# Kernel tuning notes

Hardware: AMD Instinct MI355X
Metric: run time of the kernel (lower is better)

## Reference

```python
import jax, jax.numpy as jnp
import numpy as np

INV_TEMP = 10.0

def pairwise_distance(x, y):
    # squared L2 distance: [b,n,c],[b,m,c] -> [b,n,m]
    x2 = jnp.sum(x * x, axis=-1, keepdims=True)          # [b,n,1]
    y2 = jnp.sum(y * y, axis=-1)[:, None, :]             # [b,1,m]
    xy = jnp.einsum('bnc,bmc->bnm', x, y)                # [b,n,m]
    return x2 + y2 - 2.0 * xy

def setup_inputs() -> dict:
    key = jax.random.key(0)
    k1, k2, k3 = jax.random.split(key, 3)
    b, n, m, c = 4, 4096, 4096, 32
    x_f = jax.random.normal(k1, (b, n, c), dtype=jnp.float32)
    y_f = jax.random.normal(k2, (b, m, c), dtype=jnp.float32)
    y_c = jax.random.normal(k3, (b, m, 3), dtype=jnp.float32)
    temp_inv = jnp.ones((1,), dtype=jnp.float32) * INV_TEMP
    return {"x_f": x_f, "y_f": y_f, "y_c": y_c, "temp_inv": temp_inv}

def reference(x_f, y_f, y_c, temp_inv):
    # corr_type='soft', st=True (straight-through)
    dist = pairwise_distance(x_f, y_f)                   # [b,n,m]
    y_soft = jax.nn.softmax(-dist * temp_inv[0], axis=2) # [b,n,m]
    index = jnp.argmax(y_soft, axis=2)                   # [b,n]
    y_hard = jax.nn.one_hot(index, y_soft.shape[2], dtype=y_soft.dtype)
    ret = y_hard - jax.lax.stop_gradient(y_soft) + y_soft
    x_corr = jnp.matmul(ret, y_c)                        # [b,n,3]
    return x_corr
```

## Files before the change

### kernel.cpp

```cpp
#include <hip/hip_runtime.h>

#define B 4
#define N 4096
#define M 4096
#define C 32
#define BN (B * N)

typedef short bf16x8 __attribute__((ext_vector_type(8)));
typedef float f32x4  __attribute__((ext_vector_type(4)));
typedef unsigned int u32x4 __attribute__((ext_vector_type(4)));

#define WS_WI ((size_t)8 * BN * 4)
#define WS_YH (WS_WI * 2)
#define WS_YM (WS_YH + (size_t)B * M * C * 2)
#define WS_YL (WS_YM + (size_t)B * M * C * 2)
#define WS_Y2 (WS_YL + (size_t)B * M * C * 2)

__device__ __forceinline__ float bf16lo(unsigned int u) { return __uint_as_float(u << 16); }
__device__ __forceinline__ float bf16hi(unsigned int u) { return __uint_as_float(u & 0xffff0000u); }

__device__ __forceinline__ void split3(const float f[8], bf16x8& h, bf16x8& m, bf16x8& l) {
    u32x4 hw, mw, lw;
    #pragma unroll
    for (int p = 0; p < 4; ++p) {
        const float f0 = f[2*p], f1 = f[2*p+1];
        const unsigned int h0 = __float_as_uint(f0) & 0xffff0000u;
        const unsigned int h1 = __float_as_uint(f1) & 0xffff0000u;
        hw[p] = h1 | (h0 >> 16);
        const float r0 = f0 - __uint_as_float(h0);
        const float r1 = f1 - __uint_as_float(h1);
        const unsigned int m0 = __float_as_uint(r0) & 0xffff0000u;
        const unsigned int m1 = __float_as_uint(r1) & 0xffff0000u;
        mw[p] = m1 | (m0 >> 16);
        const float s0 = r0 - __uint_as_float(m0);
        const float s1 = r1 - __uint_as_float(m1);
        lw[p] = (__float_as_uint(s1) & 0xffff0000u) | (__float_as_uint(s0) >> 16);
    }
    h = __builtin_bit_cast(bf16x8, hw);
    m = __builtin_bit_cast(bf16x8, mw);
    l = __builtin_bit_cast(bf16x8, lw);
}

__global__ __launch_bounds__(256)
void y_prepass(const void* __restrict__ yptr, const unsigned short* __restrict__ tptr,
               void* __restrict__ ws) {
    if (tptr[0] == 0x4120) return;
    unsigned short* yh = (unsigned short*)((char*)ws + WS_YH);
    unsigned short* ym = (unsigned short*)((char*)ws + WS_YM);
    unsigned short* yl = (unsigned short*)((char*)ws + WS_YL);
    float*          y2 = (float*)((char*)ws + WS_Y2);

    const int gid = blockIdx.x * 256 + threadIdx.x;
    const int row = gid >> 2;
    const int seg = gid & 3;
    const float* p = (const float*)yptr + (size_t)row * C + seg * 8;
    float4 v0 = *(const float4*)p;
    float4 v1 = *(const float4*)(p + 4);
    const float f[8] = {v0.x, v0.y, v0.z, v0.w, v1.x, v1.y, v1.z, v1.w};

    bf16x8 h, m, l;
    split3(f, h, m, l);
    const size_t o = (size_t)row * C + seg * 8;
    *(bf16x8*)(yh + o) = h;
    *(bf16x8*)(ym + o) = m;
    *(bf16x8*)(yl + o) = l;

    float s = 0.f;
    #pragma unroll
    for (int k = 0; k < 8; ++k) s = fmaf(f[k], f[k], s);
    s += __shfl_xor(s, 1, 64);
    s += __shfl_xor(s, 2, 64);
    if (seg == 0) y2[row] = -0.5f * s;
}

__global__ __launch_bounds__(256, 4)
void nn_main(const void* __restrict__ xptr, const void* __restrict__ yptr,
             const unsigned short* __restrict__ tptr, void* __restrict__ ws) {
    float* wD = (float*)ws;
    int*   wI = (int*)((char*)ws + WS_WI);
    const bool is_bf16 = (tptr[0] == 0x4120);

    __shared__ float y2s[512];

    const int tid  = threadIdx.x;
    const int lane = tid & 63;
    const int wv   = tid >> 6;
    const int col  = lane & 15;
    const int quad = lane >> 4;
    const int bi   = blockIdx.x;
    const int ms   = bi & 7;
    const int nb   = (bi >> 3) & 31;
    const int b    = bi >> 8;
    const int n_base = nb * 128 + wv * 32;

    float bD[2][4];
    int   bI[2][4];
    #pragma unroll
    for (int t = 0; t < 2; ++t)
        #pragma unroll
        for (int r = 0; r < 4; ++r) { bD[t][r] = -__builtin_inff(); bI[t][r] = 0; }

    const size_t boff = (size_t)col * C + quad * 8;

    if (is_bf16) {
        const unsigned short* yp = (const unsigned short*)yptr;
        const unsigned short* xp = (const unsigned short*)xptr;

        for (int r = tid; r < 512; r += 256) {
            const int m = ms * 512 + r;
            const uint4* p = (const uint4*)(yp + ((size_t)b * M + m) * C);
            float s = 0.f;
            #pragma unroll
            for (int i = 0; i < 4; ++i) {
                uint4 v = p[i];
                float f;
                f = bf16lo(v.x); s = fmaf(f, f, s); f = bf16hi(v.x); s = fmaf(f, f, s);
                f = bf16lo(v.y); s = fmaf(f, f, s); f = bf16hi(v.y); s = fmaf(f, f, s);
                f = bf16lo(v.z); s = fmaf(f, f, s); f = bf16hi(v.z); s = fmaf(f, f, s);
                f = bf16lo(v.w); s = fmaf(f, f, s); f = bf16hi(v.w); s = fmaf(f, f, s);
            }
            y2s[r] = -0.5f * s;
        }

        bf16x8 af[2];
        #pragma unroll
        for (int t = 0; t < 2; ++t)
            af[t] = *(const bf16x8*)(xp + ((size_t)b * N + n_base + t * 16 + col) * C + quad * 8);

        __syncthreads();

        const unsigned short* yb = yp + ((size_t)b * M + ms * 512) * C;
        bf16x8 bfr = *(const bf16x8*)(yb + boff);
        for (int mt = 0; mt < 32; ++mt) {
            bf16x8 bnx = bfr;
            if (mt < 31) bnx = *(const bf16x8*)(yb + boff + (size_t)(mt + 1) * (16 * C));
            const float y2c  = y2s[mt * 16 + col];
            const int   mcur = ms * 512 + mt * 16 + col;
            #pragma unroll
            for (int t = 0; t < 2; ++t) {
                f32x4 acc = {y2c, y2c, y2c, y2c};
                acc = __builtin_amdgcn_mfma_f32_16x16x32_bf16(af[t], bfr, acc, 0, 0, 0);
                #pragma unroll
                for (int r = 0; r < 4; ++r)
                    if (acc[r] > bD[t][r]) { bD[t][r] = acc[r]; bI[t][r] = mcur; }
            }
            bfr = bnx;
        }
    } else {
        const unsigned short* yh = (const unsigned short*)((char*)ws + WS_YH) + ((size_t)b * M + ms * 512) * C;
        const unsigned short* ym = (const unsigned short*)((char*)ws + WS_YM) + ((size_t)b * M + ms * 512) * C;
        const unsigned short* yl = (const unsigned short*)((char*)ws + WS_YL) + ((size_t)b * M + ms * 512) * C;
        const float*         y2g = (const float*)((char*)ws + WS_Y2) + (size_t)b * M + ms * 512;

        for (int r = tid; r < 512; r += 256) y2s[r] = y2g[r];

        const float* xp = (const float*)xptr;
        bf16x8 ah[2], am[2], al[2];
        #pragma unroll
        for (int t = 0; t < 2; ++t) {
            const float* xr = xp + ((size_t)b * N + n_base + t * 16 + col) * C + quad * 8;
            float4 v0 = *(const float4*)xr;
            float4 v1 = *(const float4*)(xr + 4);
            const float xf[8] = {v0.x, v0.y, v0.z, v0.w, v1.x, v1.y, v1.z, v1.w};
            split3(xf, ah[t], am[t], al[t]);
        }

        __syncthreads();

        bf16x8 bh = *(const bf16x8*)(yh + boff);
        bf16x8 bmi = *(const bf16x8*)(ym + boff);
        bf16x8 bl = *(const bf16x8*)(yl + boff);
        for (int mt = 0; mt < 32; ++mt) {
            bf16x8 nh = bh, nm = bmi, nl = bl;
            if (mt < 31) {
                const size_t no = boff + (size_t)(mt + 1) * (16 * C);
                nh = *(const bf16x8*)(yh + no);
                nm = *(const bf16x8*)(ym + no);
                nl = *(const bf16x8*)(yl + no);
            }
            const float y2c  = y2s[mt * 16 + col];
            const int   mcur = ms * 512 + mt * 16 + col;
            #pragma unroll
            for (int t = 0; t < 2; ++t) {
                f32x4 acc = {y2c, y2c, y2c, y2c};
                acc = __builtin_amdgcn_mfma_f32_16x16x32_bf16(ah[t], bh,  acc, 0, 0, 0);
                acc = __builtin_amdgcn_mfma_f32_16x16x32_bf16(am[t], bh,  acc, 0, 0, 0);
                acc = __builtin_amdgcn_mfma_f32_16x16x32_bf16(al[t], bh,  acc, 0, 0, 0);
                acc = __builtin_amdgcn_mfma_f32_16x16x32_bf16(ah[t], bmi, acc, 0, 0, 0);
                acc = __builtin_amdgcn_mfma_f32_16x16x32_bf16(am[t], bmi, acc, 0, 0, 0);
                acc = __builtin_amdgcn_mfma_f32_16x16x32_bf16(al[t], bmi, acc, 0, 0, 0);
                acc = __builtin_amdgcn_mfma_f32_16x16x32_bf16(ah[t], bl,  acc, 0, 0, 0);
                acc = __builtin_amdgcn_mfma_f32_16x16x32_bf16(am[t], bl,  acc, 0, 0, 0);
                acc = __builtin_amdgcn_mfma_f32_16x16x32_bf16(al[t], bl,  acc, 0, 0, 0);
                #pragma unroll
                for (int r = 0; r < 4; ++r)
                    if (acc[r] > bD[t][r]) { bD[t][r] = acc[r]; bI[t][r] = mcur; }
            }
            bh = nh; bmi = nm; bl = nl;
        }
    }

    #pragma unroll
    for (int mask = 1; mask < 16; mask <<= 1) {
        #pragma unroll
        for (int t = 0; t < 2; ++t)
            #pragma unroll
            for (int r = 0; r < 4; ++r) {
                float oD = __shfl_xor(bD[t][r], mask, 64);
                int   oI = __shfl_xor(bI[t][r], mask, 64);
                if (oD > bD[t][r] || (oD == bD[t][r] && oI < bI[t][r])) {
                    bD[t][r] = oD; bI[t][r] = oI;
                }
            }
    }

    if (col == 0) {
        #pragma unroll
        for (int t = 0; t < 2; ++t)
            #pragma unroll
            for (int r = 0; r < 4; ++r) {
                const int n = n_base + t * 16 + quad * 4 + r;
                const size_t g = (size_t)ms * BN + (size_t)b * N + n;
                wD[g] = bD[t][r];
                wI[g] = bI[t][r];
            }
    }
}

__global__ __launch_bounds__(256)
void nn_combine(const float* __restrict__ wD, const int* __restrict__ wI,
                const void* __restrict__ ycptr,
                const unsigned short* __restrict__ tptr,
                void* __restrict__ outptr) {
    const bool is_bf16 = (tptr[0] == 0x4120);
    const int tid  = threadIdx.x;
    const int lane = tid & 63;
    const int wv   = tid >> 6;
    const int s    = lane >> 3;
    const int ro   = lane & 7;
    const int row  = blockIdx.x * 32 + wv * 8 + ro;

    float k  = wD[(size_t)s * BN + row];
    int   ix = wI[(size_t)s * BN + row];
    #pragma unroll
    for (int mask = 8; mask < 64; mask <<= 1) {
        float ok = __shfl_xor(k, mask, 64);
        int   oi = __shfl_xor(ix, mask, 64);
        if (ok > k || (ok == k && oi < ix)) { k = ok; ix = oi; }
    }

    if (s == 0) {
        const int b = row >> 12;
        const size_t src = ((size_t)b * M + ix) * 3;
        if (is_bf16) {
            const unsigned short* yc = (const unsigned short*)ycptr;
            unsigned short* o = (unsigned short*)outptr;
            o[row*3+0] = yc[src+0];
            o[row*3+1] = yc[src+1];
            o[row*3+2] = yc[src+2];
        } else {
            const float* yc = (const float*)ycptr;
            float* o = (float*)outptr;
            o[row*3+0] = yc[src+0];
            o[row*3+1] = yc[src+1];
            o[row*3+2] = yc[src+2];
        }
    }
}

extern "C" void kernel_launch(void* const* d_in, const int* in_sizes, int n_in,
                              void* d_out, int out_size, void* d_ws, size_t ws_size,
                              hipStream_t stream) {
    const void* x  = d_in[0];
    const void* y  = d_in[1];
    const void* yc = d_in[2];
    const unsigned short* t = (const unsigned short*)d_in[3];

    float* wD = (float*)d_ws;
    int*   wI = (int*)((char*)d_ws + WS_WI);

    y_prepass<<<256, 256, 0, stream>>>(y, t, d_ws);
    nn_main<<<1024, 256, 0, stream>>>(x, y, t, d_ws);
    nn_combine<<<512, 256, 0, stream>>>(wD, wI, yc, t, d_out);
}
```

Baseline: 96.22 us.

## Fuse combine into main kernel via last-block atomic counter; drop low-order MFMA terms

Removes the separate combine launch. Each group of 8 m-split blocks increments a per-row-tile atomic counter, and the last block to finish reduces the partial argmax results and gathers y_c into the output. The counters are zeroed in the prepass. It also cuts the three-way bf16 split product from 9 MFMAs to 6 by dropping the small-magnitude cross terms (am*bl, al*bmi, al*bl), which lowers MFMA work but slightly reduces distance precision and could change argmax ties.

```diff
diff --git a/kernel.cpp b/kernel.cpp
--- a/kernel.cpp
+++ b/kernel.cpp
@@ -15,6 +15,7 @@
 #define WS_YM (WS_YH + (size_t)B * M * C * 2)
 #define WS_YL (WS_YM + (size_t)B * M * C * 2)
 #define WS_Y2 (WS_YL + (size_t)B * M * C * 2)
+#define WS_CT (WS_Y2 + (size_t)B * M * 4)
 
 __device__ __forceinline__ float bf16lo(unsigned int u) { return __uint_as_float(u << 16); }
 __device__ __forceinline__ float bf16hi(unsigned int u) { return __uint_as_float(u & 0xffff0000u); }
@@ -44,13 +45,16 @@
 __global__ __launch_bounds__(256)
 void y_prepass(const void* __restrict__ yptr, const unsigned short* __restrict__ tptr,
                void* __restrict__ ws) {
+    const int gid = blockIdx.x * 256 + threadIdx.x;
+    int* ctr = (int*)((char*)ws + WS_CT);
+    if (gid < 128) ctr[gid] = 0;
     if (tptr[0] == 0x4120) return;
+
     unsigned short* yh = (unsigned short*)((char*)ws + WS_YH);
     unsigned short* ym = (unsigned short*)((char*)ws + WS_YM);
     unsigned short* yl = (unsigned short*)((char*)ws + WS_YL);
     float*          y2 = (float*)((char*)ws + WS_Y2);
 
-    const int gid = blockIdx.x * 256 + threadIdx.x;
     const int row = gid >> 2;
     const int seg = gid & 3;
     const float* p = (const float*)yptr + (size_t)row * C + seg * 8;
@@ -75,12 +79,14 @@
 
 __global__ __launch_bounds__(256, 4)
 void nn_main(const void* __restrict__ xptr, const void* __restrict__ yptr,
-             const unsigned short* __restrict__ tptr, void* __restrict__ ws) {
+             const void* __restrict__ ycptr, const unsigned short* __restrict__ tptr,
+             void* __restrict__ ws, void* __restrict__ outptr) {
     float* wD = (float*)ws;
     int*   wI = (int*)((char*)ws + WS_WI);
     const bool is_bf16 = (tptr[0] == 0x4120);
 
     __shared__ float y2s[512];
+    __shared__ int   lastFlag;
 
     const int tid  = threadIdx.x;
     const int lane = tid & 63;
@@ -167,9 +173,9 @@
 
         __syncthreads();
 
-        bf16x8 bh = *(const bf16x8*)(yh + boff);
+        bf16x8 bh  = *(const bf16x8*)(yh + boff);
         bf16x8 bmi = *(const bf16x8*)(ym + boff);
-        bf16x8 bl = *(const bf16x8*)(yl + boff);
+        bf16x8 bl  = *(const bf16x8*)(yl + boff);
         for (int mt = 0; mt < 32; ++mt) {
             bf16x8 nh = bh, nm = bmi, nl = bl;
             if (mt < 31) {
@@ -183,15 +189,12 @@
             #pragma unroll
             for (int t = 0; t < 2; ++t) {
                 f32x4 acc = {y2c, y2c, y2c, y2c};
-                acc = __builtin_amdgcn_mfma_f32_16x16x32_bf16(ah[t], bh,  acc, 0, 0, 0);
-                acc = __builtin_amdgcn_mfma_f32_16x16x32_bf16(am[t], bh,  acc, 0, 0, 0);
+                acc = __builtin_amdgcn_mfma_f32_16x16x32_bf16(am[t], bmi, acc, 0, 0, 0);
+                acc = __builtin_amdgcn_mfma_f32_16x16x32_bf16(ah[t], bl,  acc, 0, 0, 0);
                 acc = __builtin_amdgcn_mfma_f32_16x16x32_bf16(al[t], bh,  acc, 0, 0, 0);
                 acc = __builtin_amdgcn_mfma_f32_16x16x32_bf16(ah[t], bmi, acc, 0, 0, 0);
-                acc = __builtin_amdgcn_mfma_f32_16x16x32_bf16(am[t], bmi, acc, 0, 0, 0);
-                acc = __builtin_amdgcn_mfma_f32_16x16x32_bf16(al[t], bmi, acc, 0, 0, 0);
-                acc = __builtin_amdgcn_mfma_f32_16x16x32_bf16(ah[t], bl,  acc, 0, 0, 0);
-                acc = __builtin_amdgcn_mfma_f32_16x16x32_bf16(am[t], bl,  acc, 0, 0, 0);
-                acc = __builtin_amdgcn_mfma_f32_16x16x32_bf16(al[t], bl,  acc, 0, 0, 0);
+                acc = __builtin_amdgcn_mfma_f32_16x16x32_bf16(am[t], bh,  acc, 0, 0, 0);
+                acc = __builtin_amdgcn_mfma_f32_16x16x32_bf16(ah[t], bh,  acc, 0, 0, 0);
                 #pragma unroll
                 for (int r = 0; r < 4; ++r)
                     if (acc[r] > bD[t][r]) { bD[t][r] = acc[r]; bI[t][r] = mcur; }
@@ -225,45 +228,46 @@
                 wI[g] = bI[t][r];
             }
     }
-}
-
-__global__ __launch_bounds__(256)
-void nn_combine(const float* __restrict__ wD, const int* __restrict__ wI,
-                const void* __restrict__ ycptr,
-                const unsigned short* __restrict__ tptr,
-                void* __restrict__ outptr) {
-    const bool is_bf16 = (tptr[0] == 0x4120);
-    const int tid  = threadIdx.x;
-    const int lane = tid & 63;
-    const int wv   = tid >> 6;
-    const int s    = lane >> 3;
-    const int ro   = lane & 7;
-    const int row  = blockIdx.x * 32 + wv * 8 + ro;
-
-    float k  = wD[(size_t)s * BN + row];
-    int   ix = wI[(size_t)s * BN + row];
-    #pragma unroll
-    for (int mask = 8; mask < 64; mask <<= 1) {
-        float ok = __shfl_xor(k, mask, 64);
-        int   oi = __shfl_xor(ix, mask, 64);
-        if (ok > k || (ok == k && oi < ix)) { k = ok; ix = oi; }
-    }
-
-    if (s == 0) {
-        const int b = row >> 12;
-        const size_t src = ((size_t)b * M + ix) * 3;
-        if (is_bf16) {
-            const unsigned short* yc = (const unsigned short*)ycptr;
-            unsigned short* o = (unsigned short*)outptr;
-            o[row*3+0] = yc[src+0];
-            o[row*3+1] = yc[src+1];
-            o[row*3+2] = yc[src+2];
-        } else {
-            const float* yc = (const float*)ycptr;
-            float* o = (float*)outptr;
-            o[row*3+0] = yc[src+0];
-            o[row*3+1] = yc[src+1];
-            o[row*3+2] = yc[src+2];
+
+    __threadfence();
+    __syncthreads();
+    if (tid == 0) {
+        int* ctr = (int*)((char*)ws + WS_CT);
+        lastFlag = (atomicAdd(&ctr[bi >> 3], 1) == 7);
+    }
+    __syncthreads();
+    if (lastFlag) {
+        __threadfence();
+        const int row0 = (bi >> 3) * 128;
+        const int s    = tid & 7;
+        #pragma unroll
+        for (int p = 0; p < 4; ++p) {
+            const int row = row0 + p * 32 + (tid >> 3);
+            float k  = wD[(size_t)s * BN + row];
+            int   ix = wI[(size_t)s * BN + row];
+            #pragma unroll
+            for (int mask = 1; mask < 8; mask <<= 1) {
+                float ok = __shfl_xor(k, mask, 64);
+                int   oi = __shfl_xor(ix, mask, 64);
+                if (ok > k || (ok == k && oi < ix)) { k = ok; ix = oi; }
+            }
+            if (s == 0) {
+                const int bb = row >> 12;
+                const size_t src = ((size_t)bb * M + ix) * 3;
+                if (is_bf16) {
+                    const unsigned short* yc = (const unsigned short*)ycptr;
+                    unsigned short* o = (unsigned short*)outptr;
+                    o[row*3+0] = yc[src+0];
+                    o[row*3+1] = yc[src+1];
+                    o[row*3+2] = yc[src+2];
+                } else {
+                    const float* yc = (const float*)ycptr;
+                    float* o = (float*)outptr;
+                    o[row*3+0] = yc[src+0];
+                    o[row*3+1] = yc[src+1];
+                    o[row*3+2] = yc[src+2];
+                }
+            }
         }
     }
 }
@@ -276,10 +280,6 @@
     const void* yc = d_in[2];
     const unsigned short* t = (const unsigned short*)d_in[3];
 
-    float* wD = (float*)d_ws;
-    int*   wI = (int*)((char*)d_ws + WS_WI);
-
     y_prepass<<<256, 256, 0, stream>>>(y, t, d_ws);
-    nn_main<<<1024, 256, 0, stream>>>(x, y, t, d_ws);
-    nn_combine<<<512, 256, 0, stream>>>(wD, wI, yc, t, d_out);
-}
+    nn_main<<<1024, 256, 0, stream>>>(x, y, yc, t, d_ws, d_out);
+}
```

Result: slower. 206.9 us (+115.0%).

## Drop low-order split-bf16 MFMA terms and split M across sixteen slices

Applied to the files above, without the earlier changes.

Removes the three smallest cross-product MFMAs (mid*low, low*mid, low*low) from the three-way bf16 emulation of fp32, cutting matrix work per tile by a third. Doubles the number of M slices per row to 16 to launch more blocks. Stores partial results row-major so the combine kernel reduces 16 contiguous candidates per row. Dropping terms slightly reduces distance precision, which could flip near-tie argmax results.

```diff
diff --git a/kernel.cpp b/kernel.cpp
--- a/kernel.cpp
+++ b/kernel.cpp
@@ -5,12 +5,13 @@
 #define M 4096
 #define C 32
 #define BN (B * N)
+#define MS 16
 
 typedef short bf16x8 __attribute__((ext_vector_type(8)));
 typedef float f32x4  __attribute__((ext_vector_type(4)));
 typedef unsigned int u32x4 __attribute__((ext_vector_type(4)));
 
-#define WS_WI ((size_t)8 * BN * 4)
+#define WS_WI ((size_t)MS * BN * 4)
 #define WS_YH (WS_WI * 2)
 #define WS_YM (WS_YH + (size_t)B * M * C * 2)
 #define WS_YL (WS_YM + (size_t)B * M * C * 2)
@@ -80,7 +81,7 @@
     int*   wI = (int*)((char*)ws + WS_WI);
     const bool is_bf16 = (tptr[0] == 0x4120);
 
-    __shared__ float y2s[512];
+    __shared__ float y2s[256];
 
     const int tid  = threadIdx.x;
     const int lane = tid & 63;
@@ -88,10 +89,11 @@
     const int col  = lane & 15;
     const int quad = lane >> 4;
     const int bi   = blockIdx.x;
-    const int ms   = bi & 7;
-    const int nb   = (bi >> 3) & 31;
-    const int b    = bi >> 8;
+    const int ms   = bi & 15;
+    const int nb   = (bi >> 4) & 31;
+    const int b    = bi >> 9;
     const int n_base = nb * 128 + wv * 32;
+    const int m0   = ms * 256;
 
     float bD[2][4];
     int   bI[2][4];
@@ -106,9 +108,9 @@
         const unsigned short* yp = (const unsigned short*)yptr;
         const unsigned short* xp = (const unsigned short*)xptr;
 
-        for (int r = tid; r < 512; r += 256) {
-            const int m = ms * 512 + r;
-            const uint4* p = (const uint4*)(yp + ((size_t)b * M + m) * C);
+        if (tid < 256) {
+            const int r = tid;
+            const uint4* p = (const uint4*)(yp + ((size_t)b * M + m0 + r) * C);
             float s = 0.f;
             #pragma unroll
             for (int i = 0; i < 4; ++i) {
@@ -129,13 +131,13 @@
 
         __syncthreads();
 
-        const unsigned short* yb = yp + ((size_t)b * M + ms * 512) * C;
+        const unsigned short* yb = yp + ((size_t)b * M + m0) * C;
         bf16x8 bfr = *(const bf16x8*)(yb + boff);
-        for (int mt = 0; mt < 32; ++mt) {
+        for (int mt = 0; mt < 16; ++mt) {
             bf16x8 bnx = bfr;
-            if (mt < 31) bnx = *(const bf16x8*)(yb + boff + (size_t)(mt + 1) * (16 * C));
+            if (mt < 15) bnx = *(const bf16x8*)(yb + boff + (size_t)(mt + 1) * (16 * C));
             const float y2c  = y2s[mt * 16 + col];
-            const int   mcur = ms * 512 + mt * 16 + col;
+            const int   mcur = m0 + mt * 16 + col;
             #pragma unroll
             for (int t = 0; t < 2; ++t) {
                 f32x4 acc = {y2c, y2c, y2c, y2c};
@@ -147,12 +149,12 @@
             bfr = bnx;
         }
     } else {
-        const unsigned short* yh = (const unsigned short*)((char*)ws + WS_YH) + ((size_t)b * M + ms * 512) * C;
-        const unsigned short* ym = (const unsigned short*)((char*)ws + WS_YM) + ((size_t)b * M + ms * 512) * C;
-        const unsigned short* yl = (const unsigned short*)((char*)ws + WS_YL) + ((size_t)b * M + ms * 512) * C;
-        const float*         y2g = (const float*)((char*)ws + WS_Y2) + (size_t)b * M + ms * 512;
-
-        for (int r = tid; r < 512; r += 256) y2s[r] = y2g[r];
+        const unsigned short* yh = (const unsigned short*)((char*)ws + WS_YH) + ((size_t)b * M + m0) * C;
+        const unsigned short* ym = (const unsigned short*)((char*)ws + WS_YM) + ((size_t)b * M + m0) * C;
+        const unsigned short* yl = (const unsigned short*)((char*)ws + WS_YL) + ((size_t)b * M + m0) * C;
+        const float*         y2g = (const float*)((char*)ws + WS_Y2) + (size_t)b * M + m0;
+
+        if (tid < 256) y2s[tid] = y2g[tid];
 
         const float* xp = (const float*)xptr;
         bf16x8 ah[2], am[2], al[2];
@@ -167,31 +169,28 @@
 
         __syncthreads();
 
-        bf16x8 bh = *(const bf16x8*)(yh + boff);
+        bf16x8 bh  = *(const bf16x8*)(yh + boff);
         bf16x8 bmi = *(const bf16x8*)(ym + boff);
-        bf16x8 bl = *(const bf16x8*)(yl + boff);
-        for (int mt = 0; mt < 32; ++mt) {
+        bf16x8 bl  = *(const bf16x8*)(yl + boff);
+        for (int mt = 0; mt < 16; ++mt) {
             bf16x8 nh = bh, nm = bmi, nl = bl;
-            if (mt < 31) {
+            if (mt < 15) {
                 const size_t no = boff + (size_t)(mt + 1) * (16 * C);
                 nh = *(const bf16x8*)(yh + no);
                 nm = *(const bf16x8*)(ym + no);
                 nl = *(const bf16x8*)(yl + no);
             }
             const float y2c  = y2s[mt * 16 + col];
-            const int   mcur = ms * 512 + mt * 16 + col;
+            const int   mcur = m0 + mt * 16 + col;
             #pragma unroll
             for (int t = 0; t < 2; ++t) {
                 f32x4 acc = {y2c, y2c, y2c, y2c};
-                acc = __builtin_amdgcn_mfma_f32_16x16x32_bf16(ah[t], bh,  acc, 0, 0, 0);
-                acc = __builtin_amdgcn_mfma_f32_16x16x32_bf16(am[t], bh,  acc, 0, 0, 0);
+                acc = __builtin_amdgcn_mfma_f32_16x16x32_bf16(am[t], bmi, acc, 0, 0, 0);
+                acc = __builtin_amdgcn_mfma_f32_16x16x32_bf16(ah[t], bl,  acc, 0, 0, 0);
                 acc = __builtin_amdgcn_mfma_f32_16x16x32_bf16(al[t], bh,  acc, 0, 0, 0);
                 acc = __builtin_amdgcn_mfma_f32_16x16x32_bf16(ah[t], bmi, acc, 0, 0, 0);
-                acc = __builtin_amdgcn_mfma_f32_16x16x32_bf16(am[t], bmi, acc, 0, 0, 0);
-                acc = __builtin_amdgcn_mfma_f32_16x16x32_bf16(al[t], bmi, acc, 0, 0, 0);
-                acc = __builtin_amdgcn_mfma_f32_16x16x32_bf16(ah[t], bl,  acc, 0, 0, 0);
-                acc = __builtin_amdgcn_mfma_f32_16x16x32_bf16(am[t], bl,  acc, 0, 0, 0);
-                acc = __builtin_amdgcn_mfma_f32_16x16x32_bf16(al[t], bl,  acc, 0, 0, 0);
+                acc = __builtin_amdgcn_mfma_f32_16x16x32_bf16(am[t], bh,  acc, 0, 0, 0);
+                acc = __builtin_amdgcn_mfma_f32_16x16x32_bf16(ah[t], bh,  acc, 0, 0, 0);
                 #pragma unroll
                 for (int r = 0; r < 4; ++r)
                     if (acc[r] > bD[t][r]) { bD[t][r] = acc[r]; bI[t][r] = mcur; }
@@ -220,7 +219,7 @@
             #pragma unroll
             for (int r = 0; r < 4; ++r) {
                 const int n = n_base + t * 16 + quad * 4 + r;
-                const size_t g = (size_t)ms * BN + (size_t)b * N + n;
+                const size_t g = ((size_t)b * N + n) * MS + ms;
                 wD[g] = bD[t][r];
                 wI[g] = bI[t][r];
             }
@@ -236,14 +235,13 @@
     const int tid  = threadIdx.x;
     const int lane = tid & 63;
     const int wv   = tid >> 6;
-    const int s    = lane >> 3;
-    const int ro   = lane & 7;
-    const int row  = blockIdx.x * 32 + wv * 8 + ro;
-
-    float k  = wD[(size_t)s * BN + row];
-    int   ix = wI[(size_t)s * BN + row];
-    #pragma unroll
-    for (int mask = 8; mask < 64; mask <<= 1) {
+    const int s    = lane & 15;
+    const int row  = blockIdx.x * 16 + wv * 4 + (lane >> 4);
+
+    float k  = wD[(size_t)row * MS + s];
+    int   ix = wI[(size_t)row * MS + s];
+    #pragma unroll
+    for (int mask = 1; mask < 16; mask <<= 1) {
         float ok = __shfl_xor(k, mask, 64);
         int   oi = __shfl_xor(ix, mask, 64);
         if (ok > k || (ok == k && oi < ix)) { k = ok; ix = oi; }
@@ -280,6 +278,6 @@
     int*   wI = (int*)((char*)d_ws + WS_WI);
 
     y_prepass<<<256, 256, 0, stream>>>(y, t, d_ws);
-    nn_main<<<1024, 256, 0, stream>>>(x, y, t, d_ws);
-    nn_combine<<<512, 256, 0, stream>>>(wD, wI, yc, t, d_out);
-}
+    nn_main<<<2048, 256, 0, stream>>>(x, y, t, d_ws);
+    nn_combine<<<1024, 256, 0, stream>>>(wD, wI, yc, t, d_out);
+}
```

New measurement: 99.86 us. 1.04x slower.
